# Kernel optimization log

Hardware: AMD Instinct MI355X
Metric: run time of the kernel (lower is better)

Reference implementation:

```python
import jax, jax.numpy as jnp
import numpy as np

N, T, D, H = 32, 1024, 1152, 16
DH = D // H            # 72
MLP = int(D * 4.0)     # 4608
EPS = 1e-6


def setup_inputs() -> dict:
    key = jax.random.key(0)
    ks = jax.random.split(key, 14)
    s = 0.02
    return {
        "x": jax.random.normal(ks[0], (N, T, D), jnp.float32),
        "c": jax.random.normal(ks[1], (N, D), jnp.float32),
        "qkv_w": jax.random.normal(ks[2], (D, 3 * D), jnp.float32) * s,
        "qkv_b": jax.random.normal(ks[3], (3 * D,), jnp.float32) * s,
        "proj_w": jax.random.normal(ks[4], (D, D), jnp.float32) * s,
        "proj_b": jax.random.normal(ks[5], (D,), jnp.float32) * s,
        "fc1_w": jax.random.normal(ks[6], (D, MLP), jnp.float32) * s,
        "fc1_b": jax.random.normal(ks[7], (MLP,), jnp.float32) * s,
        "fc2_w": jax.random.normal(ks[8], (MLP, D), jnp.float32) * s,
        "fc2_b": jax.random.normal(ks[9], (D,), jnp.float32) * s,
        "ada_w": jax.random.normal(ks[10], (D, 6 * D), jnp.float32) * s,
        "ada_b": jax.random.normal(ks[11], (6 * D,), jnp.float32) * s,
    }


def _layernorm(x):
    m = jnp.mean(x, axis=-1, keepdims=True)
    v = jnp.var(x, axis=-1, keepdims=True)
    return (x - m) * jax.lax.rsqrt(v + EPS)


def _modulate(x, shift, scale):
    # shift, scale: (N, D) broadcast over T
    return x * (1.0 + scale[:, None, :]) + shift[:, None, :]


def _attention(x, qkv_w, qkv_b, proj_w, proj_b):
    n, t, d = x.shape
    scale = DH ** (-0.5)
    qkv = x @ qkv_w + qkv_b                       # (N,T,3D)
    qkv = qkv.reshape(n, t, 3, H, DH)
    q, k, v = qkv[:, :, 0], qkv[:, :, 1], qkv[:, :, 2]  # each (N,T,H,DH)
    # Faithful to source: matmul over the LAST two dims -> per-token
    # head-vs-head attention of shape (N,T,H,H), softmax over heads.
    attn = jnp.einsum("nthd,ntkd->nthk", q * scale, k)
    attn = jax.nn.softmax(attn, axis=-1)
    out = jnp.einsum("nthk,ntkd->nthd", attn, v)  # (N,T,H,DH)
    out = out.transpose(0, 2, 1, 3).reshape(n, t, d)  # faithful scramble
    return out @ proj_w + proj_b


def _mlp(x, fc1_w, fc1_b, fc2_w, fc2_b):
    h = jax.nn.gelu(x @ fc1_w + fc1_b, approximate=False)  # exact GELU (torch default)
    return h @ fc2_w + fc2_b


def reference(x, c, qkv_w, qkv_b, proj_w, proj_b, fc1_w, fc1_b, fc2_w, fc2_b,
              ada_w, ada_b):
    ada = jax.nn.silu(c) @ ada_w + ada_b          # (N, 6D)
    (shift_msa, scale_msa, gate_msa,
     shift_mlp, scale_mlp, gate_mlp) = jnp.split(ada, 6, axis=1)
    x = x + gate_msa[:, None, :] * _attention(
        _modulate(_layernorm(x), shift_msa, scale_msa),
        qkv_w, qkv_b, proj_w, proj_b)
    x = x + gate_mlp[:, None, :] * _mlp(
        _modulate(_layernorm(x), shift_mlp, scale_mlp),
        fc1_w, fc1_b, fc2_w, fc2_b)
    return x
```

## Files before the change

kernel.cpp:

```cpp
#include <hip/hip_runtime.h>

#define DEV __device__ __forceinline__

typedef __attribute__((ext_vector_type(8))) short short8;
typedef __attribute__((ext_vector_type(8))) __bf16 bf16x8;
typedef __attribute__((ext_vector_type(4))) float f32x4;

#define TD      1024
#define DD      1152
#define HH      16
#define DHH     72
#define MLPD    4608
#define QKVN    3456
#define ADAN    6912
#define MROWS   32768

DEV unsigned short f32_to_bf16(float f) {
  unsigned int u = __float_as_uint(f);
  u += 0x7fffu + ((u >> 16) & 1u);
  return (unsigned short)(u >> 16);
}

DEV void gl16(const void* g, void* l) {
  __builtin_amdgcn_global_load_lds((__attribute__((address_space(1))) void*)g,
                                   (__attribute__((address_space(3))) void*)l,
                                   16, 0, 0);
}

DEV bf16x8 zero_bf16x8() {
  short8 z = {0, 0, 0, 0, 0, 0, 0, 0};
  return __builtin_bit_cast(bf16x8, z);
}

DEV float gelu_exact(float v) {
  return 0.5f * v * (1.0f + erff(v * 0.70710678118654752f));
}

__global__ __launch_bounds__(256) void wtrans_kernel(const float* __restrict__ W,
                                                     unsigned short* __restrict__ Wt,
                                                     int K, int N) {
  __shared__ unsigned short tile[32][33];
  const int nb = blockIdx.x * 32, kb = blockIdx.y * 32;
  const int tx = threadIdx.x, ty = threadIdx.y;
  #pragma unroll
  for (int i = ty; i < 32; i += 8)
    tile[i][tx] = f32_to_bf16(W[(size_t)(kb + i) * N + nb + tx]);
  __syncthreads();
  #pragma unroll
  for (int i = ty; i < 32; i += 8)
    Wt[(size_t)(nb + i) * K + kb + tx] = tile[tx][i];
}

__global__ __launch_bounds__(256) void ada_kernel(const float* __restrict__ c,
                                                  const float* __restrict__ ada_w,
                                                  const float* __restrict__ ada_b,
                                                  float* __restrict__ ada_out) {
  __shared__ float sc[DD];
  const int n = blockIdx.y;
  const int col = blockIdx.x * 256 + threadIdx.x;
  for (int i = threadIdx.x; i < DD; i += 256) {
    float v = c[(size_t)n * DD + i];
    sc[i] = v / (1.0f + __expf(-v));
  }
  __syncthreads();
  float acc = ada_b[col];
  #pragma unroll 8
  for (int k = 0; k < DD; ++k)
    acc += sc[k] * ada_w[(size_t)k * ADAN + col];
  ada_out[(size_t)n * ADAN + col] = acc;
}

__global__ __launch_bounds__(256) void ln_mod_kernel(const float* __restrict__ X,
                                                     const float* __restrict__ ada,
                                                     int soff,
                                                     unsigned short* __restrict__ out) {
  const int row = blockIdx.x;
  const int batch = row >> 10;
  const float* xr = X + (size_t)row * DD;
  const int t = threadIdx.x;

  float4 v0 = reinterpret_cast<const float4*>(xr)[t];
  float4 v1 = make_float4(0.f, 0.f, 0.f, 0.f);
  const bool has2 = (t < 32);
  if (has2) v1 = reinterpret_cast<const float4*>(xr)[256 + t];

  float s  = v0.x + v0.y + v0.z + v0.w + v1.x + v1.y + v1.z + v1.w;
  float sq = v0.x*v0.x + v0.y*v0.y + v0.z*v0.z + v0.w*v0.w
           + v1.x*v1.x + v1.y*v1.y + v1.z*v1.z + v1.w*v1.w;
  #pragma unroll
  for (int m = 1; m < 64; m <<= 1) {
    s  += __shfl_xor(s, m);
    sq += __shfl_xor(sq, m);
  }
  __shared__ float red[8];
  const int wv = t >> 6;
  if ((t & 63) == 0) { red[wv] = s; red[4 + wv] = sq; }
  __syncthreads();
  s  = red[0] + red[1] + red[2] + red[3];
  sq = red[4] + red[5] + red[6] + red[7];
  const float mean = s * (1.0f / 1152.0f);
  const float var  = sq * (1.0f / 1152.0f) - mean * mean;
  const float rstd = rsqrtf(var + 1e-6f);

  const float* shp = ada + (size_t)batch * ADAN + soff;
  const float* scp = shp + DD;
  unsigned short* orow = out + (size_t)row * DD;

  {
    const int col = t * 4;
    ushort4 o4;
    o4.x = f32_to_bf16((v0.x - mean) * rstd * (1.0f + scp[col + 0]) + shp[col + 0]);
    o4.y = f32_to_bf16((v0.y - mean) * rstd * (1.0f + scp[col + 1]) + shp[col + 1]);
    o4.z = f32_to_bf16((v0.z - mean) * rstd * (1.0f + scp[col + 2]) + shp[col + 2]);
    o4.w = f32_to_bf16((v0.w - mean) * rstd * (1.0f + scp[col + 3]) + shp[col + 3]);
    reinterpret_cast<ushort4*>(orow)[t] = o4;
  }
  if (has2) {
    const int col = 1024 + t * 4;
    ushort4 o4;
    o4.x = f32_to_bf16((v1.x - mean) * rstd * (1.0f + scp[col + 0]) + shp[col + 0]);
    o4.y = f32_to_bf16((v1.y - mean) * rstd * (1.0f + scp[col + 1]) + shp[col + 1]);
    o4.z = f32_to_bf16((v1.z - mean) * rstd * (1.0f + scp[col + 2]) + shp[col + 2]);
    o4.w = f32_to_bf16((v1.w - mean) * rstd * (1.0f + scp[col + 3]) + shp[col + 3]);
    reinterpret_cast<ushort4*>(orow)[256 + t] = o4;
  }
}

template <int EPI>
__global__ __launch_bounds__(256) void gemm128(const unsigned short* __restrict__ A,
                                               const unsigned short* __restrict__ Bt,
                                               const float* __restrict__ bias,
                                               const float* __restrict__ ada, int ada_off,
                                               const float* __restrict__ resid,
                                               unsigned short* __restrict__ out_bf,
                                               float* __restrict__ out_f,
                                               int N, int K) {
  __shared__ unsigned short lds[2][8192];
  const int tid = threadIdx.x;
  const int bn = blockIdx.x, bm = blockIdx.y;
  const int lane = tid & 63, w = tid >> 6;
  const int wm = w >> 1, wn = w & 1;
  const int l15 = lane & 15, lg = lane >> 4;

  const unsigned short* Abase = A + (size_t)bm * 128 * K;
  const unsigned short* Bbase = Bt + (size_t)bn * 128 * K;
  const int c1 = tid, c2 = tid + 256;
  const size_t a1 = (size_t)(c1 >> 2) * K + (c1 & 3) * 8;
  const size_t a2 = (size_t)(c2 >> 2) * K + (c2 & 3) * 8;

  f32x4 acc[4][4];
  #pragma unroll
  for (int m = 0; m < 4; ++m)
    #pragma unroll
    for (int nn = 0; nn < 4; ++nn)
      acc[m][nn] = (f32x4){0.f, 0.f, 0.f, 0.f};

  const int nkt = K >> 5;

#define STAGE(buf, kt) do {                                              \
    const size_t ko = (size_t)(kt) * 32;                                 \
    gl16(Abase + a1 + ko, &lds[buf][c1 * 8]);                            \
    gl16(Abase + a2 + ko, &lds[buf][c2 * 8]);                            \
    gl16(Bbase + a1 + ko, &lds[buf][4096 + c1 * 8]);                     \
    gl16(Bbase + a2 + ko, &lds[buf][4096 + c2 * 8]);                     \
  } while (0)

  STAGE(0, 0);
  for (int kt = 0; kt < nkt; ++kt) {
    __syncthreads();
    if (kt + 1 < nkt) STAGE((kt + 1) & 1, kt + 1);
    const unsigned short* la = lds[kt & 1];
    const unsigned short* lb = la + 4096;
    bf16x8 af[4], bfv[4];
    #pragma unroll
    for (int m = 0; m < 4; ++m)
      af[m] = *(const bf16x8*)&la[(wm * 64 + m * 16 + l15) * 32 + lg * 8];
    #pragma unroll
    for (int nn = 0; nn < 4; ++nn)
      bfv[nn] = *(const bf16x8*)&lb[(wn * 64 + nn * 16 + l15) * 32 + lg * 8];
    #pragma unroll
    for (int m = 0; m < 4; ++m)
      #pragma unroll
      for (int nn = 0; nn < 4; ++nn)
        acc[m][nn] = __builtin_amdgcn_mfma_f32_16x16x32_bf16(af[m], bfv[nn], acc[m][nn], 0, 0, 0);
  }
#undef STAGE

  const int batch = (bm * 128) >> 10;
  const size_t row0 = (size_t)bm * 128 + wm * 64;
  const int col0 = bn * 128 + wn * 64;
  #pragma unroll
  for (int nn = 0; nn < 4; ++nn) {
    const int colg = col0 + nn * 16 + l15;
    const float bv = bias[colg];
    float g = 0.0f;
    if constexpr (EPI == 1 || EPI == 3) g = ada[(size_t)batch * ADAN + ada_off + colg];
    #pragma unroll
    for (int m = 0; m < 4; ++m) {
      #pragma unroll
      for (int r = 0; r < 4; ++r) {
        const size_t idx = (row0 + m * 16 + lg * 4 + r) * (size_t)N + colg;
        const float v = acc[m][nn][r] + bv;
        if constexpr (EPI == 0)      out_bf[idx] = f32_to_bf16(v);
        else if constexpr (EPI == 2) out_bf[idx] = f32_to_bf16(gelu_exact(v));
        else if constexpr (EPI == 1) out_f[idx] = resid[idx] + g * v;
        else                         out_f[idx] = out_f[idx] + g * v;
      }
    }
  }
}

__global__ __launch_bounds__(256) void attn_kernel(const unsigned short* __restrict__ qkv,
                                                   unsigned short* __restrict__ y) {
  const int tid = threadIdx.x, w = tid >> 6, lane = tid & 63;
  const int l15 = lane & 15, lg = lane >> 4;
  const int tok = blockIdx.x * 4 + w;
  const int n = tok >> 10, t = tok & 1023;

  __shared__ unsigned short Pl[4][16 * 32];
  __shared__ unsigned short Vl[4][16 * 80];

  for (int i = lane; i < 16 * 32; i += 64)
    if ((i & 31) >= 16) Pl[w][i] = 0;

  const size_t rowb = (size_t)tok * QKVN;
  const float scale = 0.11785113019775793f;

  bf16x8 aq[3];
  #pragma unroll
  for (int kk = 0; kk < 3; ++kk) {
    const int d0 = kk * 32 + lg * 8;
    aq[kk] = (d0 < DHH) ? *(const bf16x8*)&qkv[rowb + l15 * DHH + d0] : zero_bf16x8();
  }

  for (int c = lane; c < 144; c += 64) {
    const int r = c / 9, cc = (c % 9) * 8;
    *(short8*)&Vl[w][r * 80 + cc] = *(const short8*)&qkv[rowb + 2 * DD + r * DHH + cc];
  }

  f32x4 s = (f32x4){0.f, 0.f, 0.f, 0.f};
  #pragma unroll
  for (int kk = 0; kk < 3; ++kk) {
    const int d0 = kk * 32 + lg * 8;
    bf16x8 bk = (d0 < DHH) ? *(const bf16x8*)&qkv[rowb + DD + l15 * DHH + d0] : zero_bf16x8();
    s = __builtin_amdgcn_mfma_f32_16x16x32_bf16(aq[kk], bk, s, 0, 0, 0);
  }

  float p[4], mx[4], ssum[4];
  #pragma unroll
  for (int r = 0; r < 4; ++r) { p[r] = s[r] * scale; mx[r] = p[r]; }
  #pragma unroll
  for (int mk = 1; mk <= 8; mk <<= 1)
    #pragma unroll
    for (int r = 0; r < 4; ++r) mx[r] = fmaxf(mx[r], __shfl_xor(mx[r], mk));
  #pragma unroll
  for (int r = 0; r < 4; ++r) { p[r] = __expf(p[r] - mx[r]); ssum[r] = p[r]; }
  #pragma unroll
  for (int mk = 1; mk <= 8; mk <<= 1)
    #pragma unroll
    for (int r = 0; r < 4; ++r) ssum[r] += __shfl_xor(ssum[r], mk);

  #pragma unroll
  for (int r = 0; r < 4; ++r)
    Pl[w][(lg * 4 + r) * 32 + l15] = f32_to_bf16(p[r] / ssum[r]);

  bf16x8 pa = *(const bf16x8*)&Pl[w][l15 * 32 + lg * 8];
  const int kb = (lg & 1) * 8;
  f32x4 o[5];
  #pragma unroll
  for (int df = 0; df < 5; ++df) {
    short8 bvv;
    #pragma unroll
    for (int j = 0; j < 8; ++j)
      bvv[j] = (short)Vl[w][(kb + j) * 80 + df * 16 + l15];
    o[df] = __builtin_amdgcn_mfma_f32_16x16x32_bf16(
        pa, __builtin_bit_cast(bf16x8, bvv), (f32x4){0.f, 0.f, 0.f, 0.f}, 0, 0, 0);
  }

  unsigned short* yb = y + (size_t)n * (TD * DD);
  #pragma unroll
  for (int df = 0; df < 5; ++df) {
    const int d = df * 16 + l15;
    if (d < DHH) {
      #pragma unroll
      for (int r = 0; r < 4; ++r) {
        const int h = lg * 4 + r;
        yb[h * 73728 + t * DHH + d] = f32_to_bf16(o[df][r]);
      }
    }
  }
}

extern "C" void kernel_launch(void* const* d_in, const int* in_sizes, int n_in,
                              void* d_out, int out_size, void* d_ws, size_t ws_size,
                              hipStream_t stream) {
  (void)in_sizes; (void)n_in; (void)out_size; (void)ws_size;
  const float* x      = (const float*)d_in[0];
  const float* c      = (const float*)d_in[1];
  const float* qkv_w  = (const float*)d_in[2];
  const float* qkv_b  = (const float*)d_in[3];
  const float* proj_w = (const float*)d_in[4];
  const float* proj_b = (const float*)d_in[5];
  const float* fc1_w  = (const float*)d_in[6];
  const float* fc1_b  = (const float*)d_in[7];
  const float* fc2_w  = (const float*)d_in[8];
  const float* fc2_b  = (const float*)d_in[9];
  const float* ada_w  = (const float*)d_in[10];
  const float* ada_b  = (const float*)d_in[11];
  float* out = (float*)d_out;

  char* ws = (char*)d_ws;
  unsigned short* hbuf    = (unsigned short*)ws;
  unsigned short* qkvbuf  = hbuf;
  unsigned short* attnbuf = hbuf + (size_t)MROWS * QKVN;
  size_t off = 301989888ull;
  unsigned short* xm    = (unsigned short*)(ws + off); off += 75497472ull;
  unsigned short* wtq   = (unsigned short*)(ws + off); off += 7962624ull;
  unsigned short* wtp   = (unsigned short*)(ws + off); off += 2654208ull;
  unsigned short* wtf1  = (unsigned short*)(ws + off); off += 10616832ull;
  unsigned short* wtf2  = (unsigned short*)(ws + off); off += 10616832ull;
  float*          adab  = (float*)(ws + off); off += 884736ull;

  const dim3 tb(32, 8);
  hipLaunchKernelGGL(wtrans_kernel, dim3(QKVN / 32, DD / 32), tb, 0, stream, qkv_w, wtq, DD, QKVN);
  hipLaunchKernelGGL(wtrans_kernel, dim3(DD / 32, DD / 32),   tb, 0, stream, proj_w, wtp, DD, DD);
  hipLaunchKernelGGL(wtrans_kernel, dim3(MLPD / 32, DD / 32), tb, 0, stream, fc1_w, wtf1, DD, MLPD);
  hipLaunchKernelGGL(wtrans_kernel, dim3(DD / 32, MLPD / 32), tb, 0, stream, fc2_w, wtf2, MLPD, DD);

  hipLaunchKernelGGL(ada_kernel, dim3(ADAN / 256, 32), dim3(256), 0, stream, c, ada_w, ada_b, adab);

  hipLaunchKernelGGL(ln_mod_kernel, dim3(MROWS), dim3(256), 0, stream, x, adab, 0, xm);

  hipLaunchKernelGGL((gemm128<0>), dim3(QKVN / 128, MROWS / 128), dim3(256), 0, stream,
                     xm, wtq, qkv_b, nullptr, 0, nullptr, qkvbuf, nullptr, QKVN, DD);

  hipLaunchKernelGGL(attn_kernel, dim3(MROWS / 4), dim3(256), 0, stream, qkvbuf, attnbuf);

  hipLaunchKernelGGL((gemm128<1>), dim3(DD / 128, MROWS / 128), dim3(256), 0, stream,
                     attnbuf, wtp, proj_b, adab, 2304, x, nullptr, out, DD, DD);

  hipLaunchKernelGGL(ln_mod_kernel, dim3(MROWS), dim3(256), 0, stream, out, adab, 3456, xm);

  hipLaunchKernelGGL((gemm128<2>), dim3(MLPD / 128, MROWS / 128), dim3(256), 0, stream,
                     xm, wtf1, fc1_b, nullptr, 0, nullptr, hbuf, nullptr, MLPD, DD);

  hipLaunchKernelGGL((gemm128<3>), dim3(DD / 128, MROWS / 128), dim3(256), 0, stream,
                     hbuf, wtf2, fc2_b, adab, 5760, nullptr, nullptr, out, DD, MLPD);
}
```

Baseline: 2.000 ms.

## Enlarge GEMM tiles to 256x128 with XCD-aware swizzle and finer pipelining

Replaces the 128x128 GEMM with a 256x128 tile (8x4 MFMA fragments per wave) in a new LDS layout. Block IDs are remapped so each XCD works on contiguous row panels for better L2 reuse. Loads are split and interleaved between MFMA groups, with explicit vmcnt waits, barriers and setprio, to overlap global-to-LDS traffic with compute. This costs more registers and LDS per block (launch bounds target 2 blocks per CU) in exchange for higher arithmetic intensity per loaded byte.

```diff
diff --git a/kernel.cpp b/kernel.cpp
--- a/kernel.cpp
+++ b/kernel.cpp
@@ -35,6 +35,13 @@
 DEV float gelu_exact(float v) {
   return 0.5f * v * (1.0f + erff(v * 0.70710678118654752f));
 }
+
+#define WAITV(n) asm volatile("s_waitcnt vmcnt(" #n ")" ::: "memory")
+#define BAR()                                  \
+  do {                                         \
+    __builtin_amdgcn_s_barrier();              \
+    __builtin_amdgcn_sched_barrier(0);         \
+  } while (0)
 
 __global__ __launch_bounds__(256) void wtrans_kernel(const float* __restrict__ W,
                                                      unsigned short* __restrict__ Wt,
@@ -127,68 +134,106 @@
 }
 
 template <int EPI>
-__global__ __launch_bounds__(256) void gemm128(const unsigned short* __restrict__ A,
-                                               const unsigned short* __restrict__ Bt,
-                                               const float* __restrict__ bias,
-                                               const float* __restrict__ ada, int ada_off,
-                                               const float* __restrict__ resid,
-                                               unsigned short* __restrict__ out_bf,
-                                               float* __restrict__ out_f,
-                                               int N, int K) {
-  __shared__ unsigned short lds[2][8192];
+__global__ __launch_bounds__(256, 2) void gemm256(
+    const unsigned short* __restrict__ A, const unsigned short* __restrict__ Bt,
+    const float* __restrict__ bias, const float* __restrict__ ada, int ada_off,
+    const float* __restrict__ resid, unsigned short* __restrict__ out_bf,
+    float* __restrict__ out_f, int N, int K, int nbn) {
+  __shared__ unsigned short lds[2][12288];
   const int tid = threadIdx.x;
-  const int bn = blockIdx.x, bm = blockIdx.y;
   const int lane = tid & 63, w = tid >> 6;
   const int wm = w >> 1, wn = w & 1;
   const int l15 = lane & 15, lg = lane >> 4;
 
-  const unsigned short* Abase = A + (size_t)bm * 128 * K;
-  const unsigned short* Bbase = Bt + (size_t)bn * 128 * K;
-  const int c1 = tid, c2 = tid + 256;
-  const size_t a1 = (size_t)(c1 >> 2) * K + (c1 & 3) * 8;
-  const size_t a2 = (size_t)(c2 >> 2) * K + (c2 & 3) * 8;
-
-  f32x4 acc[4][4];
-  #pragma unroll
-  for (int m = 0; m < 4; ++m)
+  const int bid = blockIdx.x;
+  const int xcd = bid & 7, idx = bid >> 3;
+  const int panel = idx / (nbn * 8);
+  const int rr = idx % (nbn * 8);
+  const int bn = rr >> 3;
+  const int bm = xcd * 16 + panel * 8 + (rr & 7);
+
+  const unsigned short* __restrict__ Ag = A + (size_t)bm * 256 * K;
+  const unsigned short* __restrict__ Bg = Bt + (size_t)bn * 128 * K;
+
+  int srow[4], sc16[4];
+  #pragma unroll
+  for (int i = 0; i < 4; ++i) {
+    const int gb = i * 4096 + tid * 16;
+    srow[i] = ((gb >> 9) << 3) | ((gb >> 4) & 7);
+    sc16[i] = (gb >> 7) & 3;
+  }
+
+  const int abase = wm * 4096 + ((l15 >> 3) << 8) + (lg << 6) + ((l15 & 7) << 3);
+  const int bbase = 8192 + wn * 2048 + ((l15 >> 3) << 8) + (lg << 6) + ((l15 & 7) << 3);
+
+  f32x4 acc[8][4];
+  #pragma unroll
+  for (int m = 0; m < 8; ++m)
     #pragma unroll
     for (int nn = 0; nn < 4; ++nn)
       acc[m][nn] = (f32x4){0.f, 0.f, 0.f, 0.f};
 
-  const int nkt = K >> 5;
-
-#define STAGE(buf, kt) do {                                              \
-    const size_t ko = (size_t)(kt) * 32;                                 \
-    gl16(Abase + a1 + ko, &lds[buf][c1 * 8]);                            \
-    gl16(Abase + a2 + ko, &lds[buf][c2 * 8]);                            \
-    gl16(Bbase + a1 + ko, &lds[buf][4096 + c1 * 8]);                     \
-    gl16(Bbase + a2 + ko, &lds[buf][4096 + c2 * 8]);                     \
+  const int NT = K >> 5;
+
+#define STG_A(bf_, kt_, i_) gl16(Ag + (size_t)srow[i_] * K + (kt_) * 32 + sc16[i_] * 8, \
+                                 &lds[bf_][(i_) * 2048 + tid * 8])
+#define STG_B(bf_, kt_, j_) gl16(Bg + (size_t)srow[j_] * K + (kt_) * 32 + sc16[j_] * 8, \
+                                 &lds[bf_][8192 + (j_) * 2048 + tid * 8])
+
+#define MFMA_PAIR(M0, M1)                                                                \
+  do {                                                                                   \
+    bf16x8 a0_ = *(const bf16x8*)&lb[abase + (M0) * 512];                                \
+    bf16x8 a1_ = *(const bf16x8*)&lb[abase + (M1) * 512];                                \
+    __builtin_amdgcn_s_setprio(1);                                                       \
+    acc[M0][0] = __builtin_amdgcn_mfma_f32_16x16x32_bf16(a0_, bf0, acc[M0][0], 0, 0, 0); \
+    acc[M0][1] = __builtin_amdgcn_mfma_f32_16x16x32_bf16(a0_, bf1, acc[M0][1], 0, 0, 0); \
+    acc[M0][2] = __builtin_amdgcn_mfma_f32_16x16x32_bf16(a0_, bf2, acc[M0][2], 0, 0, 0); \
+    acc[M0][3] = __builtin_amdgcn_mfma_f32_16x16x32_bf16(a0_, bf3, acc[M0][3], 0, 0, 0); \
+    acc[M1][0] = __builtin_amdgcn_mfma_f32_16x16x32_bf16(a1_, bf0, acc[M1][0], 0, 0, 0); \
+    acc[M1][1] = __builtin_amdgcn_mfma_f32_16x16x32_bf16(a1_, bf1, acc[M1][1], 0, 0, 0); \
+    acc[M1][2] = __builtin_amdgcn_mfma_f32_16x16x32_bf16(a1_, bf2, acc[M1][2], 0, 0, 0); \
+    acc[M1][3] = __builtin_amdgcn_mfma_f32_16x16x32_bf16(a1_, bf3, acc[M1][3], 0, 0, 0); \
+    __builtin_amdgcn_s_setprio(0);                                                       \
   } while (0)
 
-  STAGE(0, 0);
-  for (int kt = 0; kt < nkt; ++kt) {
-    __syncthreads();
-    if (kt + 1 < nkt) STAGE((kt + 1) & 1, kt + 1);
-    const unsigned short* la = lds[kt & 1];
-    const unsigned short* lb = la + 4096;
-    bf16x8 af[4], bfv[4];
-    #pragma unroll
-    for (int m = 0; m < 4; ++m)
-      af[m] = *(const bf16x8*)&la[(wm * 64 + m * 16 + l15) * 32 + lg * 8];
-    #pragma unroll
-    for (int nn = 0; nn < 4; ++nn)
-      bfv[nn] = *(const bf16x8*)&lb[(wn * 64 + nn * 16 + l15) * 32 + lg * 8];
-    #pragma unroll
-    for (int m = 0; m < 4; ++m)
-      #pragma unroll
-      for (int nn = 0; nn < 4; ++nn)
-        acc[m][nn] = __builtin_amdgcn_mfma_f32_16x16x32_bf16(af[m], bfv[nn], acc[m][nn], 0, 0, 0);
-  }
-#undef STAGE
-
-  const int batch = (bm * 128) >> 10;
-  const size_t row0 = (size_t)bm * 128 + wm * 64;
+  STG_B(0, 0, 0); STG_B(0, 0, 1);
+  STG_A(0, 0, 0); STG_A(0, 0, 2);
+  STG_A(0, 0, 1); STG_A(0, 0, 3);
+
+  for (int kt = 0; kt < NT; ++kt) {
+    const int cb = kt & 1, nbuf = cb ^ 1;
+    const unsigned short* lb = lds[cb];
+    if (kt + 1 < NT) {
+      STG_B(nbuf, kt + 1, 0); STG_B(nbuf, kt + 1, 1);
+      WAITV(4);
+    } else {
+      WAITV(2);
+    }
+    BAR();
+    bf16x8 bf0 = *(const bf16x8*)&lb[bbase];
+    bf16x8 bf1 = *(const bf16x8*)&lb[bbase + 512];
+    bf16x8 bf2 = *(const bf16x8*)&lb[bbase + 1024];
+    bf16x8 bf3 = *(const bf16x8*)&lb[bbase + 1536];
+    MFMA_PAIR(0, 1);
+    if (kt + 1 < NT) { STG_A(nbuf, kt + 1, 0); STG_A(nbuf, kt + 1, 2); }
+    MFMA_PAIR(2, 3);
+    if (kt + 1 < NT) {
+      STG_A(nbuf, kt + 1, 1); STG_A(nbuf, kt + 1, 3);
+      WAITV(6);
+    } else {
+      WAITV(0);
+    }
+    BAR();
+    MFMA_PAIR(4, 5);
+    MFMA_PAIR(6, 7);
+  }
+#undef STG_A
+#undef STG_B
+#undef MFMA_PAIR
+
+  const size_t row0 = (size_t)bm * 256 + wm * 128;
   const int col0 = bn * 128 + wn * 64;
+  const int batch = (int)(row0 >> 10);
   #pragma unroll
   for (int nn = 0; nn < 4; ++nn) {
     const int colg = col0 + nn * 16 + l15;
@@ -196,15 +241,15 @@
     float g = 0.0f;
     if constexpr (EPI == 1 || EPI == 3) g = ada[(size_t)batch * ADAN + ada_off + colg];
     #pragma unroll
-    for (int m = 0; m < 4; ++m) {
+    for (int mf = 0; mf < 8; ++mf) {
       #pragma unroll
       for (int r = 0; r < 4; ++r) {
-        const size_t idx = (row0 + m * 16 + lg * 4 + r) * (size_t)N + colg;
-        const float v = acc[m][nn][r] + bv;
-        if constexpr (EPI == 0)      out_bf[idx] = f32_to_bf16(v);
-        else if constexpr (EPI == 2) out_bf[idx] = f32_to_bf16(gelu_exact(v));
-        else if constexpr (EPI == 1) out_f[idx] = resid[idx] + g * v;
-        else                         out_f[idx] = out_f[idx] + g * v;
+        const size_t oidx = (row0 + mf * 16 + lg * 4 + r) * (size_t)N + colg;
+        const float v = acc[mf][nn][r] + bv;
+        if constexpr (EPI == 0)      out_bf[oidx] = f32_to_bf16(v);
+        else if constexpr (EPI == 2) out_bf[oidx] = f32_to_bf16(gelu_exact(v));
+        else if constexpr (EPI == 1) out_f[oidx] = resid[oidx] + g * v;
+        else                         out_f[oidx] = out_f[oidx] + g * v;
       }
     }
   }
@@ -331,19 +376,19 @@
 
   hipLaunchKernelGGL(ln_mod_kernel, dim3(MROWS), dim3(256), 0, stream, x, adab, 0, xm);
 
-  hipLaunchKernelGGL((gemm128<0>), dim3(QKVN / 128, MROWS / 128), dim3(256), 0, stream,
-                     xm, wtq, qkv_b, nullptr, 0, nullptr, qkvbuf, nullptr, QKVN, DD);
+  hipLaunchKernelGGL((gemm256<0>), dim3(128 * 27), dim3(256), 0, stream,
+                     xm, wtq, qkv_b, nullptr, 0, nullptr, qkvbuf, nullptr, QKVN, DD, 27);
 
   hipLaunchKernelGGL(attn_kernel, dim3(MROWS / 4), dim3(256), 0, stream, qkvbuf, attnbuf);
 
-  hipLaunchKernelGGL((gemm128<1>), dim3(DD / 128, MROWS / 128), dim3(256), 0, stream,
-                     attnbuf, wtp, proj_b, adab, 2304, x, nullptr, out, DD, DD);
+  hipLaunchKernelGGL((gemm256<1>), dim3(128 * 9), dim3(256), 0, stream,
+                     attnbuf, wtp, proj_b, adab, 2304, x, nullptr, out, DD, DD, 9);
 
   hipLaunchKernelGGL(ln_mod_kernel, dim3(MROWS), dim3(256), 0, stream, out, adab, 3456, xm);
 
-  hipLaunchKernelGGL((gemm128<2>), dim3(MLPD / 128, MROWS / 128), dim3(256), 0, stream,
-                     xm, wtf1, fc1_b, nullptr, 0, nullptr, hbuf, nullptr, MLPD, DD);
-
-  hipLaunchKernelGGL((gemm128<3>), dim3(DD / 128, MROWS / 128), dim3(256), 0, stream,
-                     hbuf, wtf2, fc2_b, adab, 5760, nullptr, nullptr, out, DD, MLPD);
-}
+  hipLaunchKernelGGL((gemm256<2>), dim3(128 * 36), dim3(256), 0, stream,
+                     xm, wtf1, fc1_b, nullptr, 0, nullptr, hbuf, nullptr, MLPD, DD, 36);
+
+  hipLaunchKernelGGL((gemm256<3>), dim3(128 * 9), dim3(256), 0, stream,
+                     hbuf, wtf2, fc2_b, adab, 5760, nullptr, nullptr, out, DD, MLPD, 9);
+}
```

New measurement: 2.325 ms. 16.3% more time.

## Swizzle GEMM block order per XCD and reorganize LDS tile layout

Applied to the files above, without the earlier changes.

The GEMM kernel now takes a 1D grid and remaps block IDs so that each XCD owns a contiguous 32-row band of M tiles, walked in groups of 8 M tiles across all N tiles. This is meant to raise L2 reuse of A and B tiles within each XCD. The LDS staging layout is also permuted into 8-row by 4-k-chunk groups, so fragment reads use precomputed offsets and should hit fewer bank conflicts. The index mapping is hardcoded to 256 M tiles (MROWS/128), and the LDS permutation has to match exactly between the global_load_lds writes and the fragment reads.

```diff
diff --git a/kernel.cpp b/kernel.cpp
--- a/kernel.cpp
+++ b/kernel.cpp
@@ -134,19 +134,32 @@
                                                const float* __restrict__ resid,
                                                unsigned short* __restrict__ out_bf,
                                                float* __restrict__ out_f,
-                                               int N, int K) {
+                                               int N, int K, int nbn) {
   __shared__ unsigned short lds[2][8192];
   const int tid = threadIdx.x;
-  const int bn = blockIdx.x, bm = blockIdx.y;
   const int lane = tid & 63, w = tid >> 6;
   const int wm = w >> 1, wn = w & 1;
   const int l15 = lane & 15, lg = lane >> 4;
 
-  const unsigned short* Abase = A + (size_t)bm * 128 * K;
-  const unsigned short* Bbase = Bt + (size_t)bn * 128 * K;
+  const int bid = blockIdx.x;
+  const int xcd = bid & 7;
+  const int i = bid >> 3;
+  const int g = i / (8 * nbn);
+  const int rem = i - g * (8 * nbn);
+  const int bn = rem >> 3;
+  const int bm = xcd * 32 + g * 8 + (rem & 7);
+
+  const unsigned short* __restrict__ Abase = A + (size_t)bm * 128 * K;
+  const unsigned short* __restrict__ Bbase = Bt + (size_t)bn * 128 * K;
+
   const int c1 = tid, c2 = tid + 256;
-  const size_t a1 = (size_t)(c1 >> 2) * K + (c1 & 3) * 8;
-  const size_t a2 = (size_t)(c2 >> 2) * K + (c2 & 3) * 8;
+  const int r1 = ((c1 >> 5) << 3) | (c1 & 7), k1 = (c1 >> 3) & 3;
+  const int r2 = ((c2 >> 5) << 3) | (c2 & 7), k2 = (c2 >> 3) & 3;
+  const size_t a1 = (size_t)r1 * K + k1 * 8;
+  const size_t a2 = (size_t)r2 * K + k2 * 8;
+
+  const int abase = (wm * 8 + (l15 >> 3)) * 256 + (lg << 6) + ((l15 & 7) << 3);
+  const int bbase = 4096 + (wn * 8 + (l15 >> 3)) * 256 + (lg << 6) + ((l15 & 7) << 3);
 
   f32x4 acc[4][4];
   #pragma unroll
@@ -170,14 +183,14 @@
     __syncthreads();
     if (kt + 1 < nkt) STAGE((kt + 1) & 1, kt + 1);
     const unsigned short* la = lds[kt & 1];
-    const unsigned short* lb = la + 4096;
+    const unsigned short* lb = la;
     bf16x8 af[4], bfv[4];
     #pragma unroll
     for (int m = 0; m < 4; ++m)
-      af[m] = *(const bf16x8*)&la[(wm * 64 + m * 16 + l15) * 32 + lg * 8];
+      af[m] = *(const bf16x8*)&la[abase + m * 512];
     #pragma unroll
     for (int nn = 0; nn < 4; ++nn)
-      bfv[nn] = *(const bf16x8*)&lb[(wn * 64 + nn * 16 + l15) * 32 + lg * 8];
+      bfv[nn] = *(const bf16x8*)&lb[bbase + nn * 512];
     #pragma unroll
     for (int m = 0; m < 4; ++m)
       #pragma unroll
@@ -193,8 +206,8 @@
   for (int nn = 0; nn < 4; ++nn) {
     const int colg = col0 + nn * 16 + l15;
     const float bv = bias[colg];
-    float g = 0.0f;
-    if constexpr (EPI == 1 || EPI == 3) g = ada[(size_t)batch * ADAN + ada_off + colg];
+    float g2 = 0.0f;
+    if constexpr (EPI == 1 || EPI == 3) g2 = ada[(size_t)batch * ADAN + ada_off + colg];
     #pragma unroll
     for (int m = 0; m < 4; ++m) {
       #pragma unroll
@@ -203,8 +216,8 @@
         const float v = acc[m][nn][r] + bv;
         if constexpr (EPI == 0)      out_bf[idx] = f32_to_bf16(v);
         else if constexpr (EPI == 2) out_bf[idx] = f32_to_bf16(gelu_exact(v));
-        else if constexpr (EPI == 1) out_f[idx] = resid[idx] + g * v;
-        else                         out_f[idx] = out_f[idx] + g * v;
+        else if constexpr (EPI == 1) out_f[idx] = resid[idx] + g2 * v;
+        else                         out_f[idx] = out_f[idx] + g2 * v;
       }
     }
   }
@@ -331,19 +344,19 @@
 
   hipLaunchKernelGGL(ln_mod_kernel, dim3(MROWS), dim3(256), 0, stream, x, adab, 0, xm);
 
-  hipLaunchKernelGGL((gemm128<0>), dim3(QKVN / 128, MROWS / 128), dim3(256), 0, stream,
-                     xm, wtq, qkv_b, nullptr, 0, nullptr, qkvbuf, nullptr, QKVN, DD);
+  hipLaunchKernelGGL((gemm128<0>), dim3(256 * 27), dim3(256), 0, stream,
+                     xm, wtq, qkv_b, nullptr, 0, nullptr, qkvbuf, nullptr, QKVN, DD, 27);
 
   hipLaunchKernelGGL(attn_kernel, dim3(MROWS / 4), dim3(256), 0, stream, qkvbuf, attnbuf);
 
-  hipLaunchKernelGGL((gemm128<1>), dim3(DD / 128, MROWS / 128), dim3(256), 0, stream,
-                     attnbuf, wtp, proj_b, adab, 2304, x, nullptr, out, DD, DD);
+  hipLaunchKernelGGL((gemm128<1>), dim3(256 * 9), dim3(256), 0, stream,
+                     attnbuf, wtp, proj_b, adab, 2304, x, nullptr, out, DD, DD, 9);
 
   hipLaunchKernelGGL(ln_mod_kernel, dim3(MROWS), dim3(256), 0, stream, out, adab, 3456, xm);
 
-  hipLaunchKernelGGL((gemm128<2>), dim3(MLPD / 128, MROWS / 128), dim3(256), 0, stream,
-                     xm, wtf1, fc1_b, nullptr, 0, nullptr, hbuf, nullptr, MLPD, DD);
-
-  hipLaunchKernelGGL((gemm128<3>), dim3(DD / 128, MROWS / 128), dim3(256), 0, stream,
-                     hbuf, wtf2, fc2_b, adab, 5760, nullptr, nullptr, out, DD, MLPD);
-}
+  hipLaunchKernelGGL((gemm128<2>), dim3(256 * 36), dim3(256), 0, stream,
+                     xm, wtf1, fc1_b, nullptr, 0, nullptr, hbuf, nullptr, MLPD, DD, 36);
+
+  hipLaunchKernelGGL((gemm128<3>), dim3(256 * 9), dim3(256), 0, stream,
+                     hbuf, wtf2, fc2_b, adab, 5760, nullptr, nullptr, out, DD, MLPD, 9);
+}
```

After: 2.371 ms. 1.19x slower.

## Enlarge GEMM tile to 256x128 with XOR-swizzled LDS and explicit vmcnt waits

Applied to the files above, without the earlier changes.

Replaces the 128x128 GEMM with a 256x128 tile in which each wave computes 128x64, raising arithmetic intensity per staged byte. LDS layout is XOR-swizzled to reduce bank conflicts, and __syncthreads is replaced by raw barriers plus explicit vmcnt waits so the next-stage prefetch stays in flight. MFMA issue is wrapped in s_setprio. Risks are higher register pressure from 32 accumulators, which may lower occupancy, and fewer blocks in the grid.

```diff
diff --git a/kernel.cpp b/kernel.cpp
--- a/kernel.cpp
+++ b/kernel.cpp
@@ -35,6 +35,8 @@
 DEV float gelu_exact(float v) {
   return 0.5f * v * (1.0f + erff(v * 0.70710678118654752f));
 }
+
+#define WAITV(n) asm volatile("s_waitcnt vmcnt(" #n ")" ::: "memory")
 
 __global__ __launch_bounds__(256) void wtrans_kernel(const float* __restrict__ W,
                                                      unsigned short* __restrict__ Wt,
@@ -127,84 +129,108 @@
 }
 
 template <int EPI>
-__global__ __launch_bounds__(256) void gemm128(const unsigned short* __restrict__ A,
-                                               const unsigned short* __restrict__ Bt,
-                                               const float* __restrict__ bias,
-                                               const float* __restrict__ ada, int ada_off,
-                                               const float* __restrict__ resid,
-                                               unsigned short* __restrict__ out_bf,
-                                               float* __restrict__ out_f,
-                                               int N, int K) {
-  __shared__ unsigned short lds[2][8192];
+__global__ __launch_bounds__(256) void gemm2p(const unsigned short* __restrict__ A,
+                                              const unsigned short* __restrict__ Bt,
+                                              const float* __restrict__ bias,
+                                              const float* __restrict__ ada, int ada_off,
+                                              const float* __restrict__ resid,
+                                              unsigned short* __restrict__ out_bf,
+                                              float* __restrict__ out_f,
+                                              int N, int K) {
+  __shared__ unsigned short lds[2][12288];
   const int tid = threadIdx.x;
-  const int bn = blockIdx.x, bm = blockIdx.y;
   const int lane = tid & 63, w = tid >> 6;
   const int wm = w >> 1, wn = w & 1;
   const int l15 = lane & 15, lg = lane >> 4;
-
-  const unsigned short* Abase = A + (size_t)bm * 128 * K;
-  const unsigned short* Bbase = Bt + (size_t)bn * 128 * K;
-  const int c1 = tid, c2 = tid + 256;
-  const size_t a1 = (size_t)(c1 >> 2) * K + (c1 & 3) * 8;
-  const size_t a2 = (size_t)(c2 >> 2) * K + (c2 & 3) * 8;
-
-  f32x4 acc[4][4];
-  #pragma unroll
-  for (int m = 0; m < 4; ++m)
+  const int bn = blockIdx.x, bm = blockIdx.y;
+
+  const unsigned short* __restrict__ Ag = A + (size_t)bm * 256 * K;
+  const unsigned short* __restrict__ Bg = Bt + (size_t)bn * 128 * K;
+
+  size_t aoff[4], boff[2];
+  #pragma unroll
+  for (int i = 0; i < 4; ++i) {
+    const int s = i * 256 + tid, r = s >> 2;
+    aoff[i] = (size_t)r * K + (((s & 3) ^ ((r >> 1) & 3)) * 8);
+  }
+  #pragma unroll
+  for (int j = 0; j < 2; ++j) {
+    const int s = j * 256 + tid, r = s >> 2;
+    boff[j] = (size_t)r * K + (((s & 3) ^ ((r >> 1) & 3)) * 8);
+  }
+
+  const int colp = lg ^ ((l15 >> 1) & 3);
+  const int abase = (wm * 128 + l15) * 4 + colp;
+  const int bbase = 1024 + (wn * 64 + l15) * 4 + colp;
+
+  f32x4 acc[8][4];
+  #pragma unroll
+  for (int m = 0; m < 8; ++m)
     #pragma unroll
     for (int nn = 0; nn < 4; ++nn)
       acc[m][nn] = (f32x4){0.f, 0.f, 0.f, 0.f};
 
-  const int nkt = K >> 5;
-
-#define STAGE(buf, kt) do {                                              \
-    const size_t ko = (size_t)(kt) * 32;                                 \
-    gl16(Abase + a1 + ko, &lds[buf][c1 * 8]);                            \
-    gl16(Abase + a2 + ko, &lds[buf][c2 * 8]);                            \
-    gl16(Bbase + a1 + ko, &lds[buf][4096 + c1 * 8]);                     \
-    gl16(Bbase + a2 + ko, &lds[buf][4096 + c2 * 8]);                     \
+  const int NC = K >> 5;
+
+#define STG(c_) do {                                            \
+    const int rc_ = (c_) & 1;                                   \
+    const size_t ko_ = (size_t)(c_) * 32;                       \
+    gl16(Ag + aoff[0] + ko_, &lds[rc_][tid * 8]);               \
+    gl16(Ag + aoff[1] + ko_, &lds[rc_][2048 + tid * 8]);        \
+    gl16(Ag + aoff[2] + ko_, &lds[rc_][4096 + tid * 8]);        \
+    gl16(Ag + aoff[3] + ko_, &lds[rc_][6144 + tid * 8]);        \
+    gl16(Bg + boff[0] + ko_, &lds[rc_][8192 + tid * 8]);        \
+    gl16(Bg + boff[1] + ko_, &lds[rc_][10240 + tid * 8]);       \
   } while (0)
 
-  STAGE(0, 0);
-  for (int kt = 0; kt < nkt; ++kt) {
-    __syncthreads();
-    if (kt + 1 < nkt) STAGE((kt + 1) & 1, kt + 1);
-    const unsigned short* la = lds[kt & 1];
-    const unsigned short* lb = la + 4096;
-    bf16x8 af[4], bfv[4];
-    #pragma unroll
-    for (int m = 0; m < 4; ++m)
-      af[m] = *(const bf16x8*)&la[(wm * 64 + m * 16 + l15) * 32 + lg * 8];
+  STG(0);
+  for (int c = 0; c < NC; ++c) {
+    __builtin_amdgcn_s_barrier();
+    if (c + 1 < NC) {
+      STG(c + 1);
+      WAITV(6);
+    } else {
+      WAITV(0);
+    }
+    __builtin_amdgcn_s_barrier();
+
+    const unsigned short* lb = lds[c & 1];
+    bf16x8 af[8], bfv[4];
+    #pragma unroll
+    for (int m = 0; m < 8; ++m)
+      af[m] = *(const bf16x8*)&lb[(abase + m * 64) * 8];
     #pragma unroll
     for (int nn = 0; nn < 4; ++nn)
-      bfv[nn] = *(const bf16x8*)&lb[(wn * 64 + nn * 16 + l15) * 32 + lg * 8];
-    #pragma unroll
-    for (int m = 0; m < 4; ++m)
+      bfv[nn] = *(const bf16x8*)&lb[(bbase + nn * 64) * 8];
+    __builtin_amdgcn_s_setprio(1);
+    #pragma unroll
+    for (int m = 0; m < 8; ++m)
       #pragma unroll
       for (int nn = 0; nn < 4; ++nn)
         acc[m][nn] = __builtin_amdgcn_mfma_f32_16x16x32_bf16(af[m], bfv[nn], acc[m][nn], 0, 0, 0);
-  }
-#undef STAGE
-
-  const int batch = (bm * 128) >> 10;
-  const size_t row0 = (size_t)bm * 128 + wm * 64;
+    __builtin_amdgcn_s_setprio(0);
+  }
+#undef STG
+
+  const size_t row0 = (size_t)bm * 256 + wm * 128;
   const int col0 = bn * 128 + wn * 64;
+  const int batch = bm >> 2;
   #pragma unroll
   for (int nn = 0; nn < 4; ++nn) {
     const int colg = col0 + nn * 16 + l15;
     const float bv = bias[colg];
-    float g = 0.0f;
-    if constexpr (EPI == 1 || EPI == 3) g = ada[(size_t)batch * ADAN + ada_off + colg];
-    #pragma unroll
-    for (int m = 0; m < 4; ++m) {
+    float g2 = 0.0f;
+    if constexpr (EPI == 1 || EPI == 3) g2 = ada[(size_t)batch * ADAN + ada_off + colg];
+    #pragma unroll
+    for (int mf = 0; mf < 8; ++mf) {
       #pragma unroll
       for (int r = 0; r < 4; ++r) {
-        const size_t idx = (row0 + m * 16 + lg * 4 + r) * (size_t)N + colg;
-        const float v = acc[m][nn][r] + bv;
+        const size_t idx = (row0 + mf * 16 + lg * 4 + r) * (size_t)N + colg;
+        const float v = acc[mf][nn][r] + bv;
         if constexpr (EPI == 0)      out_bf[idx] = f32_to_bf16(v);
         else if constexpr (EPI == 2) out_bf[idx] = f32_to_bf16(gelu_exact(v));
-        else if constexpr (EPI == 1) out_f[idx] = resid[idx] + g * v;
-        else                         out_f[idx] = out_f[idx] + g * v;
+        else if constexpr (EPI == 1) out_f[idx] = resid[idx] + g2 * v;
+        else                         out_f[idx] = out_f[idx] + g2 * v;
       }
     }
   }
@@ -331,19 +357,19 @@
 
   hipLaunchKernelGGL(ln_mod_kernel, dim3(MROWS), dim3(256), 0, stream, x, adab, 0, xm);
 
-  hipLaunchKernelGGL((gemm128<0>), dim3(QKVN / 128, MROWS / 128), dim3(256), 0, stream,
+  hipLaunchKernelGGL((gemm2p<0>), dim3(QKVN / 128, MROWS / 256), dim3(256), 0, stream,
                      xm, wtq, qkv_b, nullptr, 0, nullptr, qkvbuf, nullptr, QKVN, DD);
 
   hipLaunchKernelGGL(attn_kernel, dim3(MROWS / 4), dim3(256), 0, stream, qkvbuf, attnbuf);
 
-  hipLaunchKernelGGL((gemm128<1>), dim3(DD / 128, MROWS / 128), dim3(256), 0, stream,
+  hipLaunchKernelGGL((gemm2p<1>), dim3(DD / 128, MROWS / 256), dim3(256), 0, stream,
                      attnbuf, wtp, proj_b, adab, 2304, x, nullptr, out, DD, DD);
 
   hipLaunchKernelGGL(ln_mod_kernel, dim3(MROWS), dim3(256), 0, stream, out, adab, 3456, xm);
 
-  hipLaunchKernelGGL((gemm128<2>), dim3(MLPD / 128, MROWS / 128), dim3(256), 0, stream,
+  hipLaunchKernelGGL((gemm2p<2>), dim3(MLPD / 128, MROWS / 256), dim3(256), 0, stream,
                      xm, wtf1, fc1_b, nullptr, 0, nullptr, hbuf, nullptr, MLPD, DD);
 
-  hipLaunchKernelGGL((gemm128<3>), dim3(DD / 128, MROWS / 128), dim3(256), 0, stream,
+  hipLaunchKernelGGL((gemm2p<3>), dim3(DD / 128, MROWS / 256), dim3(256), 0, stream,
                      hbuf, wtf2, fc2_b, adab, 5760, nullptr, nullptr, out, DD, MLPD);
 }
```

Result: slower. 2.480 ms (+24.0%).
